# Performance work log

Hardware: AMD Instinct MI355X
Metric: run time of the kernel (lower is better)

## Reference

```python
import jax, jax.numpy as jnp
import numpy as np

BLOCK_SIZE = 256
N_EMBD = 384
HEAD_SIZE = 384
B = 256
T = 256


def setup_inputs() -> dict:
    key = jax.random.key(0)
    kx, kk, kq, kv = jax.random.split(key, 4)
    scale = 1.0 / np.sqrt(N_EMBD)
    x = jax.random.normal(kx, (B, T, N_EMBD), dtype=jnp.float32)
    Wk = jax.random.normal(kk, (HEAD_SIZE, N_EMBD), dtype=jnp.float32) * scale
    Wq = jax.random.normal(kq, (HEAD_SIZE, N_EMBD), dtype=jnp.float32) * scale
    Wv = jax.random.normal(kv, (HEAD_SIZE, N_EMBD), dtype=jnp.float32) * scale
    return {"x": x, "Wk": Wk, "Wq": Wq, "Wv": Wv}


def reference(x, Wk, Wq, Wv):
    # Single-head causal self-attention; equals forward_with_cache at prefill
    # (fresh cache, cache_index=0, T tokens) and forward_no_cache.
    # Linear layers are bias-free: y = x @ W.T
    k = jnp.einsum('btc,hc->bth', x, Wk)  # [B,T,H]
    q = jnp.einsum('btc,hc->bth', x, Wq)
    v = jnp.einsum('btc,hc->bth', x, Wv)
    inv_sqrt_hs = jnp.asarray(HEAD_SIZE, x.dtype) ** -0.5
    wei = jnp.einsum('bth,bsh->bts', q, k) * inv_sqrt_hs  # [B,T,T]
    causal = jnp.tril(jnp.ones((T, T), dtype=bool))
    wei = jnp.where(causal, wei, jnp.asarray(-jnp.inf, wei.dtype))
    wei = jax.nn.softmax(wei, axis=-1)
    # dropout is identity in eval mode
    out = jnp.einsum('bts,bsh->bth', wei, v)  # [B,T,H]
    return out
```

## Files before the change

### kernel.cpp

```cpp
#include <hip/hip_runtime.h>

#define B_ 256
#define T_ 256
#define C_ 384
#define H_ 384

typedef float f4 __attribute__((ext_vector_type(4)));
typedef float f32x4 __attribute__((ext_vector_type(4)));
typedef short bf8 __attribute__((ext_vector_type(8)));
typedef short s8v __attribute__((ext_vector_type(8)));
typedef short s4v __attribute__((ext_vector_type(4)));

__device__ __forceinline__ short f2bf(float f) {
  unsigned u = __builtin_bit_cast(unsigned, f);
  u += 0x7FFFu + ((u >> 16) & 1u);
  return (short)(u >> 16);
}

__device__ __forceinline__ void gload_lds16(const void* g, void* l) {
  __builtin_amdgcn_global_load_lds(
      (const __attribute__((address_space(1))) unsigned int*)g,
      (__attribute__((address_space(3))) unsigned int*)l, 16, 0, 0);
}

__global__ __launch_bounds__(256) void convert_kernel(
    const float* __restrict__ x, const float* __restrict__ wk,
    const float* __restrict__ wq, const float* __restrict__ wv,
    short* __restrict__ xb, short* __restrict__ wb) {
  const int NXG = (B_ * T_ * C_) / 8;
  const int NWG = (H_ * C_) / 8;
  const int total = NXG + 3 * NWG;
  for (int g = blockIdx.x * 256 + threadIdx.x; g < total; g += gridDim.x * 256) {
    const float* src;
    short* dst;
    if (g < NXG) {
      src = x + (size_t)g * 8;
      dst = xb + (size_t)g * 8;
    } else {
      int h = g - NXG;
      int wsel = h / NWG;
      int o = h - wsel * NWG;
      const float* wp = wsel == 0 ? wk : (wsel == 1 ? wq : wv);
      src = wp + (size_t)o * 8;
      dst = wb + (size_t)wsel * (H_ * C_) + (size_t)o * 8;
    }
    f4 f0 = *(const f4*)src;
    f4 f1 = *(const f4*)(src + 4);
    s8v r;
    r[0] = f2bf(f0[0]); r[1] = f2bf(f0[1]); r[2] = f2bf(f0[2]); r[3] = f2bf(f0[3]);
    r[4] = f2bf(f1[0]); r[5] = f2bf(f1[1]); r[6] = f2bf(f1[2]); r[7] = f2bf(f1[3]);
    *(s8v*)dst = r;
  }
}

__global__ __launch_bounds__(512, 2) void proj_gemm(
    const short* __restrict__ xb, const short* __restrict__ wb,
    short* __restrict__ kb, short* __restrict__ qbuf, short* __restrict__ vt) {
  __shared__ __align__(16) short lA[2][512 * 64];
  __shared__ __align__(16) short lB[2][128 * 64];
  const int tid = threadIdx.x;
  const int bid = blockIdx.x;
  const int swz = (bid & 7) * 144 + (bid >> 3);
  const int nb = swz % 9;
  const int mb = swz / 9;
  const int m0 = mb * 512, gn0 = nb * 128;
  const int w = tid >> 6, l = tid & 63;
  const int wrm = w >> 1, wcn = w & 1;

  auto STAGE = [&](int buf, int t) {
    const int k0 = t * 64;
#pragma unroll
    for (int j = 0; j < 8; ++j) {
      const int flat = j * 512 + tid;
      const int row = flat >> 3;
      const int colg = ((flat & 7) ^ (row & 7)) * 8;
      gload_lds16(xb + (size_t)(m0 + row) * C_ + k0 + colg,
                  (char*)&lA[buf][0] + flat * 16);
    }
#pragma unroll
    for (int j = 0; j < 2; ++j) {
      const int flat = j * 512 + tid;
      const int row = flat >> 3;
      const int colg = ((flat & 7) ^ (row & 7)) * 8;
      gload_lds16(wb + (size_t)(gn0 + row) * C_ + k0 + colg,
                  (char*)&lB[buf][0] + flat * 16);
    }
  };

  f32x4 acc[8][4] = {};
  STAGE(0, 0);
#pragma unroll
  for (int t = 0; t < 6; ++t) {
    const int cur = t & 1;
    if (t < 5) {
      STAGE(cur ^ 1, t + 1);
      asm volatile("s_waitcnt vmcnt(10)" ::: "memory");
    } else {
      asm volatile("s_waitcnt vmcnt(0)" ::: "memory");
    }
    __builtin_amdgcn_s_barrier();
    __builtin_amdgcn_sched_barrier(0);
    const short* A = &lA[cur][0];
    const short* Bt = &lB[cur][0];
#pragma unroll
    for (int ks = 0; ks < 2; ++ks) {
      const int kg = ks * 4 + (l >> 4);
      bf8 av[8], bv[4];
#pragma unroll
      for (int mt = 0; mt < 8; ++mt) {
        const int ra = wrm * 128 + mt * 16 + (l & 15);
        av[mt] = *(const bf8*)&A[ra * 64 + ((kg ^ (ra & 7)) << 3)];
      }
#pragma unroll
      for (int nt = 0; nt < 4; ++nt) {
        const int rb = wcn * 64 + nt * 16 + (l & 15);
        bv[nt] = *(const bf8*)&Bt[rb * 64 + ((kg ^ (rb & 7)) << 3)];
      }
      __builtin_amdgcn_s_setprio(1);
#pragma unroll
      for (int mt = 0; mt < 8; ++mt)
#pragma unroll
        for (int nt = 0; nt < 4; ++nt)
          acc[mt][nt] = __builtin_amdgcn_mfma_f32_16x16x32_bf16(
              av[mt], bv[nt], acc[mt][nt], 0, 0, 0);
      __builtin_amdgcn_s_setprio(0);
    }
    __builtin_amdgcn_sched_barrier(0);
    __builtin_amdgcn_s_barrier();
  }
  const int proj = nb / 3;
  const int gcb = (nb % 3) * 128 + wcn * 64 + (l & 15);
  const int tok0 = m0 + wrm * 128 + ((l >> 4) * 4);
  if (proj < 2) {
    short* dst = proj == 0 ? kb : qbuf;
#pragma unroll
    for (int mt = 0; mt < 8; ++mt)
#pragma unroll
      for (int nt = 0; nt < 4; ++nt)
#pragma unroll
        for (int r = 0; r < 4; ++r)
          dst[(size_t)(tok0 + mt * 16 + r) * H_ + gcb + nt * 16] =
              f2bf(acc[mt][nt][r]);
  } else {
    const int bb = tok0 >> 8;
    const int tl0 = tok0 & 255;
#pragma unroll
    for (int mt = 0; mt < 8; ++mt)
#pragma unroll
      for (int nt = 0; nt < 4; ++nt) {
        s4v pk;
        pk[0] = f2bf(acc[mt][nt][0]); pk[1] = f2bf(acc[mt][nt][1]);
        pk[2] = f2bf(acc[mt][nt][2]); pk[3] = f2bf(acc[mt][nt][3]);
        *(s4v*)&vt[(size_t)bb * (H_ * T_) + (size_t)(gcb + nt * 16) * T_ +
                   tl0 + mt * 16] = pk;
      }
  }
}

__global__ __launch_bounds__(256) void attn_kernel(
    const short* __restrict__ qbuf, const short* __restrict__ kb,
    const short* __restrict__ vt, float* __restrict__ out) {
  __shared__ __align__(16) char smem[40960];
  short* Kl = (short*)smem;
  short* Ql = (short*)(smem + 32768);
  short* Pl = (short*)smem;
  const int bid = blockIdx.x;
  const int swzb = (bid & 7) * 128 + (bid >> 3);
  const int b = swzb >> 2;
  const int qi = swzb & 3;
  const int t0 = qi * 64;
  const int SKV = t0 + 64;
  const int ntile = SKV >> 4;
  const int tid = threadIdx.x;
  const int w = tid >> 6, l = tid & 63;
  f32x4 sa[16] = {};
  for (int hc = 0; hc < 6; ++hc) {
    const int h0 = hc * 64;
#pragma unroll
    for (int j = 0; j < 2; ++j) {
      const int flat = j * 256 + tid;
      const int row = flat >> 3;
      const int colg = ((flat & 7) ^ (row & 7)) * 8;
      gload_lds16(qbuf + (size_t)(b * T_ + t0 + row) * H_ + h0 + colg,
                  (char*)Ql + flat * 16);
    }
    const int kiss = SKV >> 5;
    for (int j = 0; j < kiss; ++j) {
      const int flat = j * 256 + tid;
      const int row = flat >> 3;
      const int colg = ((flat & 7) ^ (row & 7)) * 8;
      gload_lds16(kb + (size_t)(b * T_ + row) * H_ + h0 + colg,
                  (char*)Kl + flat * 16);
    }
    __syncthreads();
#pragma unroll
    for (int ks = 0; ks < 2; ++ks) {
      const int kg = ks * 4 + (l >> 4);
      const int rq = w * 16 + (l & 15);
      bf8 av = *(const bf8*)&Ql[rq * 64 + ((kg ^ (rq & 7)) << 3)];
#pragma unroll
      for (int nt = 0; nt < 16; ++nt)
        if (nt < ntile) {
          const int rk = nt * 16 + (l & 15);
          bf8 bv = *(const bf8*)&Kl[rk * 64 + ((kg ^ (rk & 7)) << 3)];
          sa[nt] = __builtin_amdgcn_mfma_f32_16x16x32_bf16(av, bv, sa[nt], 0, 0, 0);
        }
    }
    __syncthreads();
  }
  const float scale = 0.05103103630798287f;
  const int rbl = w * 16 + (l >> 4) * 4;
#pragma unroll
  for (int r = 0; r < 4; ++r) {
    const int prow = rbl + r;
    const int trow = t0 + prow;
    float vv[16];
    float m = -3.0e38f;
#pragma unroll
    for (int nt = 0; nt < 16; ++nt)
      if (nt < ntile) {
        const int col = nt * 16 + (l & 15);
        float v = sa[nt][r] * scale;
        if (col > trow) v = -3.0e38f;
        vv[nt] = v;
        m = fmaxf(m, v);
      }
    m = fmaxf(m, __shfl_xor(m, 1));
    m = fmaxf(m, __shfl_xor(m, 2));
    m = fmaxf(m, __shfl_xor(m, 4));
    m = fmaxf(m, __shfl_xor(m, 8));
    float s = 0.f;
#pragma unroll
    for (int nt = 0; nt < 16; ++nt)
      if (nt < ntile) {
        vv[nt] = __expf(vv[nt] - m);
        s += vv[nt];
      }
    s += __shfl_xor(s, 1);
    s += __shfl_xor(s, 2);
    s += __shfl_xor(s, 4);
    s += __shfl_xor(s, 8);
    const float inv = 1.0f / s;
    const int sw = (prow & 7) << 3;
#pragma unroll
    for (int nt = 0; nt < 16; ++nt)
      if (nt < ntile) {
        const int col = nt * 16 + (l & 15);
        Pl[prow * 256 + (col ^ sw)] = f2bf(vv[nt] * inv);
      }
  }
  __syncthreads();
  f32x4 o[4][6] = {};
  const int nks = SKV >> 5;
  for (int ks = 0; ks < nks; ++ks) {
    const int kk = ks * 32 + (l >> 4) * 8;
    bf8 av[4];
#pragma unroll
    for (int mt = 0; mt < 4; ++mt) {
      const int rp = mt * 16 + (l & 15);
      av[mt] = *(const bf8*)&Pl[rp * 256 + (kk ^ ((rp & 7) << 3))];
    }
#pragma unroll
    for (int nt = 0; nt < 6; ++nt) {
      const int d = w * 96 + nt * 16 + (l & 15);
      bf8 bv = *(const bf8*)&vt[(size_t)b * (H_ * T_) + (size_t)d * T_ + kk];
#pragma unroll
      for (int mt = 0; mt < 4; ++mt)
        o[mt][nt] = __builtin_amdgcn_mfma_f32_16x16x32_bf16(av[mt], bv, o[mt][nt], 0, 0, 0);
    }
  }
#pragma unroll
  for (int mt = 0; mt < 4; ++mt) {
    const int tok = b * T_ + t0 + mt * 16 + (l >> 4) * 4;
#pragma unroll
    for (int nt = 0; nt < 6; ++nt) {
      const int d = w * 96 + nt * 16 + (l & 15);
#pragma unroll
      for (int r = 0; r < 4; ++r)
        out[(size_t)(tok + r) * H_ + d] = o[mt][nt][r];
    }
  }
}

extern "C" void kernel_launch(void* const* d_in, const int* in_sizes, int n_in,
                              void* d_out, int out_size, void* d_ws, size_t ws_size,
                              hipStream_t stream) {
  (void)in_sizes; (void)n_in; (void)out_size; (void)ws_size;
  const float* x = (const float*)d_in[0];
  const float* wk = (const float*)d_in[1];
  const float* wq = (const float*)d_in[2];
  const float* wv = (const float*)d_in[3];
  float* out = (float*)d_out;
  char* ws = (char*)d_ws;
  const size_t SZ = (size_t)B_ * T_ * H_ * 2;
  short* kbuf = (short*)ws;
  short* qbuf = (short*)(ws + SZ);
  short* vt   = (short*)(ws + 2 * SZ);
  short* xb = (short*)d_out;
  short* wb = (short*)((char*)d_out + SZ);
  convert_kernel<<<2048, 256, 0, stream>>>(x, wk, wq, wv, xb, wb);
  proj_gemm<<<1152, 512, 0, stream>>>(xb, wb, kbuf, qbuf, vt);
  attn_kernel<<<1024, 256, 0, stream>>>(qbuf, kbuf, vt, out);
}
```

Measured before the change: 323.6 us.

## Double-buffer K tiles in LDS, keep Q in registers, prefetch V

The attention kernel now loads its Q rows straight into registers once instead of staging them through LDS each head chunk. K chunks are double-buffered in LDS with explicit vmcnt waits and barriers so the next chunk loads while MFMAs run on the current one. V fragments for the next k-step are prefetched in registers during the PV loop, and s_setprio wraps the MFMA sections. The change raises LDS use to 64KB and register pressure, which could limit occupancy despite launch_bounds(256,2). It also always loads the full 256 K rows, even for causal tiles that need fewer.

```diff
diff --git a/kernel.cpp b/kernel.cpp
--- a/kernel.cpp
+++ b/kernel.cpp
@@ -157,13 +157,11 @@
   }
 }
 
-__global__ __launch_bounds__(256) void attn_kernel(
+__global__ __launch_bounds__(256, 2) void attn_kernel(
     const short* __restrict__ qbuf, const short* __restrict__ kb,
     const short* __restrict__ vt, float* __restrict__ out) {
-  __shared__ __align__(16) char smem[40960];
-  short* Kl = (short*)smem;
-  short* Ql = (short*)(smem + 32768);
-  short* Pl = (short*)smem;
+  __shared__ __align__(16) short Kl[2][256 * 64];
+  short* Pl = &Kl[0][0];
   const int bid = blockIdx.x;
   const int swzb = (bid & 7) * 128 + (bid >> 3);
   const int b = swzb >> 2;
@@ -171,43 +169,64 @@
   const int t0 = qi * 64;
   const int SKV = t0 + 64;
   const int ntile = SKV >> 4;
+  const int nks = SKV >> 5;
   const int tid = threadIdx.x;
   const int w = tid >> 6, l = tid & 63;
-  f32x4 sa[16] = {};
-  for (int hc = 0; hc < 6; ++hc) {
+
+  bf8 qv[6][2];
+  {
+    const short* qrow =
+        qbuf + (size_t)(b * T_ + t0 + w * 16 + (l & 15)) * H_ + (l >> 4) * 8;
+#pragma unroll
+    for (int hc = 0; hc < 6; ++hc)
+#pragma unroll
+      for (int ks = 0; ks < 2; ++ks)
+        qv[hc][ks] = *(const bf8*)(qrow + hc * 64 + ks * 32);
+  }
+
+  auto STAGE = [&](int buf, int hc) {
     const int h0 = hc * 64;
 #pragma unroll
-    for (int j = 0; j < 2; ++j) {
-      const int flat = j * 256 + tid;
-      const int row = flat >> 3;
-      const int colg = ((flat & 7) ^ (row & 7)) * 8;
-      gload_lds16(qbuf + (size_t)(b * T_ + t0 + row) * H_ + h0 + colg,
-                  (char*)Ql + flat * 16);
-    }
-    const int kiss = SKV >> 5;
-    for (int j = 0; j < kiss; ++j) {
+    for (int j = 0; j < 8; ++j) {
       const int flat = j * 256 + tid;
       const int row = flat >> 3;
       const int colg = ((flat & 7) ^ (row & 7)) * 8;
       gload_lds16(kb + (size_t)(b * T_ + row) * H_ + h0 + colg,
-                  (char*)Kl + flat * 16);
-    }
-    __syncthreads();
+                  (char*)&Kl[buf][0] + flat * 16);
+    }
+  };
+
+  f32x4 sa[16] = {};
+  STAGE(0, 0);
+#pragma unroll
+  for (int hc = 0; hc < 6; ++hc) {
+    if (hc < 5) {
+      STAGE((hc + 1) & 1, hc + 1);
+      asm volatile("s_waitcnt vmcnt(8)" ::: "memory");
+    } else {
+      asm volatile("s_waitcnt vmcnt(0)" ::: "memory");
+    }
+    __builtin_amdgcn_s_barrier();
+    __builtin_amdgcn_sched_barrier(0);
+    const short* Kb = &Kl[hc & 1][0];
 #pragma unroll
     for (int ks = 0; ks < 2; ++ks) {
       const int kg = ks * 4 + (l >> 4);
-      const int rq = w * 16 + (l & 15);
-      bf8 av = *(const bf8*)&Ql[rq * 64 + ((kg ^ (rq & 7)) << 3)];
+      __builtin_amdgcn_s_setprio(1);
 #pragma unroll
       for (int nt = 0; nt < 16; ++nt)
         if (nt < ntile) {
           const int rk = nt * 16 + (l & 15);
-          bf8 bv = *(const bf8*)&Kl[rk * 64 + ((kg ^ (rk & 7)) << 3)];
-          sa[nt] = __builtin_amdgcn_mfma_f32_16x16x32_bf16(av, bv, sa[nt], 0, 0, 0);
+          bf8 bv = *(const bf8*)&Kb[rk * 64 + ((kg ^ (rk & 7)) << 3)];
+          sa[nt] = __builtin_amdgcn_mfma_f32_16x16x32_bf16(qv[hc][ks], bv,
+                                                           sa[nt], 0, 0, 0);
         }
-    }
-    __syncthreads();
-  }
+      __builtin_amdgcn_s_setprio(0);
+    }
+    __builtin_amdgcn_sched_barrier(0);
+    __builtin_amdgcn_s_barrier();
+  }
+
   const float scale = 0.05103103630798287f;
   const int rbl = w * 16 + (l >> 4) * 4;
 #pragma unroll
@@ -250,24 +269,40 @@
       }
   }
   __syncthreads();
+
+  const size_t vbase = (size_t)b * (H_ * T_);
+  bf8 vc[6], vn[6];
+  {
+    const int kk0 = (l >> 4) * 8;
+#pragma unroll
+    for (int nt = 0; nt < 6; ++nt)
+      vc[nt] = *(const bf8*)&vt[vbase + (size_t)(w * 96 + nt * 16 + (l & 15)) * T_ + kk0];
+  }
   f32x4 o[4][6] = {};
-  const int nks = SKV >> 5;
   for (int ks = 0; ks < nks; ++ks) {
     const int kk = ks * 32 + (l >> 4) * 8;
+    if (ks + 1 < nks) {
+      const int kk2 = kk + 32;
+#pragma unroll
+      for (int nt = 0; nt < 6; ++nt)
+        vn[nt] = *(const bf8*)&vt[vbase + (size_t)(w * 96 + nt * 16 + (l & 15)) * T_ + kk2];
+    }
     bf8 av[4];
 #pragma unroll
     for (int mt = 0; mt < 4; ++mt) {
       const int rp = mt * 16 + (l & 15);
       av[mt] = *(const bf8*)&Pl[rp * 256 + (kk ^ ((rp & 7) << 3))];
     }
-#pragma unroll
-    for (int nt = 0; nt < 6; ++nt) {
-      const int d = w * 96 + nt * 16 + (l & 15);
-      bf8 bv = *(const bf8*)&vt[(size_t)b * (H_ * T_) + (size_t)d * T_ + kk];
+    __builtin_amdgcn_s_setprio(1);
+#pragma unroll
+    for (int nt = 0; nt < 6; ++nt)
 #pragma unroll
       for (int mt = 0; mt < 4; ++mt)
-        o[mt][nt] = __builtin_amdgcn_mfma_f32_16x16x32_bf16(av[mt], bv, o[mt][nt], 0, 0, 0);
-    }
+        o[mt][nt] = __builtin_amdgcn_mfma_f32_16x16x32_bf16(av[mt], vc[nt],
+                                                            o[mt][nt], 0, 0, 0);
+    __builtin_amdgcn_s_setprio(0);
+#pragma unroll
+    for (int nt = 0; nt < 6; ++nt) vc[nt] = vn[nt];
   }
 #pragma unroll
   for (int mt = 0; mt < 4; ++mt) {
```

Result: no change. 326.2 us (+0.8%).
